# Kernel tuning notes

Measured on AMD Instinct MI355X. Metric: run time of the kernel, lower is better.

## Reference

```python
import jax, jax.numpy as jnp
import numpy as np

B, Q, N_WAY, K_SHOT = 2, 75, 5, 5
C, H, W = 640, 5, 5
PROJ, HEAD_DIM = 640, 32
NUM_HEAD = PROJ // HEAD_DIM
SCALE = HEAD_DIM ** 0.5
TEMP = 12.5
ALPHAS = [2.0 ** k for k in range(-3, 2)]  # cfg.model.mmd.alphas**k, k in [-3,2)


def setup_inputs() -> dict:
    key = jax.random.key(0)
    ks = jax.random.split(key, 7)
    std = (2.0 / PROJ) ** 0.5  # torch init: normal(0, sqrt(2/(k*k*out)))
    return {
        "support_xf": jax.random.normal(ks[0], (B, N_WAY * K_SHOT, C, H, W), jnp.float32),
        "support_y": jax.random.randint(ks[1], (B, N_WAY * K_SHOT), 0, N_WAY),
        "query_xf": jax.random.normal(ks[2], (B, Q, C, H, W), jnp.float32),
        "query_y": jax.random.randint(ks[3], (B, Q), 0, N_WAY),
        "Wq": jax.random.normal(ks[4], (PROJ, C), jnp.float32) * std,
        "Wk": jax.random.normal(ks[5], (PROJ, C), jnp.float32) * std,
        "Wv": jax.random.normal(ks[6], (C, C), jnp.float32) * ((2.0 / C) ** 0.5),
    }


def _qkv(x, Wq, Wk, Wv):
    # x: [b, n, c, h, w]; 1x1 convs == channel matmuls
    b, n, c, h, w = x.shape
    xf = x.reshape(b, n, c, h * w)
    proj = lambda Wm: jnp.einsum('oc,bncp->bnop', Wm, xf)
    k = proj(Wk).reshape(b, n, NUM_HEAD, -1, h * w)                   # [b,n,nh,hd,p]
    q = proj(Wq).reshape(b, n, NUM_HEAD, -1, h * w).swapaxes(-1, -2)  # [b,n,nh,p,hd]
    v = proj(Wv).reshape(b, n, NUM_HEAD, -1, h * w).swapaxes(-1, -2)  # [b,n,nh,p,ch]
    return q, k, v


def _cross_attn(q, k, v, shortcut, dim):
    # q:[b,*,*,nh,p,hd], k:[b,*,*,nh,hd,p], v:[b,*,*,nh,p,ch] (broadcasting over q/s axes)
    attn = jax.nn.softmax((q / SCALE) @ k, axis=-1)
    out = attn @ v                                  # [b,Q,S,nh,p,ch]
    b, nq, s = out.shape[:3]
    h, w = shortcut.shape[-2:]
    out = out.swapaxes(-1, -2).reshape(b, nq, s, -1, h, w)  # [b,Q,S,c,h,w]
    return out + jnp.expand_dims(shortcut, dim)


def _sqdist(x, y):
    # squared euclidean pairwise distances over last-two dims; == cdist(x,y)**2
    xx = jnp.sum(x * x, -1)[..., :, None]
    yy = jnp.sum(y * y, -1)[..., None, :]
    d2 = xx + yy - 2.0 * jnp.einsum('...nc,...mc->...nm', x, y)
    return jnp.maximum(d2, 0.0)


def _mgk(d2):
    # multi-scale gaussian kernel: sum_a exp(-a * dist^2)
    k = jnp.exp(-ALPHAS[0] * d2)
    for a in ALPHAS[1:]:
        k = k + jnp.exp(-a * d2)
    return k


def _forward(support_xf, query_xf, query_y, Wq, Wk, Wv):
    b, q, c, h, w = query_xf.shape
    sq, sk, sv = _qkv(support_xf, Wq, Wk, Wv)
    qq_, qk_, qv_ = _qkv(query_xf, Wq, Wk, Wv)
    # support features attended by query queries (shortcut = support, broadcast over q)
    sbq = _cross_attn(qq_[:, :, None], sk[:, None], sv[:, None], support_xf, dim=1)  # [b,q,s,c,h,w]
    # query features attended by support queries (shortcut = query, broadcast over s)
    qbs = _cross_attn(sq[:, None], qk_[:, :, None], qv_[:, :, None], query_xf, dim=2)

    def regroup(t):  # [b,q,s,c,h,w] -> [b,q,n_way,k_shot*h*w,c]
        t = t.reshape(b, q, N_WAY, K_SHOT, c, h, w)
        return t.transpose(0, 1, 2, 3, 5, 6, 4).reshape(b, q, N_WAY, K_SHOT * h * w, c)

    sxf = regroup(sbq)
    qxf = regroup(qbs)
    # centering over channel dim
    sxf = sxf - sxf.mean(-1, keepdims=True)
    qxf = qxf - qxf.mean(-1, keepdims=True)

    Kss = _mgk(_sqdist(sxf, sxf))  # [b,q,n_way,N,N]
    Kqq = _mgk(_sqdist(qxf, qxf))
    Kqs = _mgk(_sqdist(sxf, qxf))

    N = K_SHOT * h * w  # num features per class-group (== num_fea_per_img)
    tot = lambda K: jnp.sum(K, (-1, -2))
    tr = lambda K: jnp.trace(K, axis1=-2, axis2=-1)  # diagonal removal (::N+1 stride)
    mmd = (tot(Kss) - tr(Kss)) / (N * (N - 1)) \
        + (tot(Kqq) - tr(Kqq)) / (N * (N - 1)) \
        - (2.0 / (N * N)) * tot(Kqs)
    mmd_dis = mmd.reshape(b * q, N_WAY)

    logp = jax.nn.log_softmax(-mmd_dis / TEMP, axis=-1)
    y = query_y.reshape(-1)
    loss = -jnp.mean(jnp.take_along_axis(logp, y[:, None], axis=1))
    return loss


def reference(support_xf, support_y, query_xf, query_y, Wq, Wk, Wv):
    return _forward(support_xf, query_xf, query_y, Wq, Wk, Wv)
```

## Files before the change

kernel.cpp:

```cpp
#include <hip/hip_runtime.h>
#include <math.h>

#define PP    25
#define CCH   640
#define NCOL  5000
#define SCALE_INV 0.17677669529663687f

#define XTB_OFF   0L
#define WB_OFF    1600000L
#define PROJB_OFF 2214400L
#define MMD_OFF   7014400L
#define ONES_OFF  7015168L
#define FEAT_OFF  7015360L
#define FEAT_PER_WAY_US 160000L
#define FEAT_PER_PAIR_US 800000L

typedef __attribute__((ext_vector_type(8)))  short          s16x8;
typedef __attribute__((ext_vector_type(8)))  unsigned short u16x8;
typedef __attribute__((ext_vector_type(4)))  unsigned short u16x4;
typedef __attribute__((ext_vector_type(16))) float          f32x16;

typedef __attribute__((address_space(1))) const unsigned int glb_u32;
typedef __attribute__((address_space(3))) unsigned int       lds_u32;

__device__ inline unsigned short f2bf(float x) {
  unsigned u = __float_as_uint(x);
  unsigned r = u + 0x7fff + ((u >> 16) & 1);
  return (unsigned short)(r >> 16);
}
__device__ inline float bf2f(unsigned short b) {
  return __uint_as_float(((unsigned)b) << 16);
}
__device__ inline unsigned cvtpk(float lo, float hi) {
  unsigned r;
  asm("v_cvt_pk_bf16_f32 %0, %1, %2" : "=v"(r) : "v"(lo), "v"(hi));
  return r;
}

__global__ __launch_bounds__(256) void t_kernel(const float* __restrict__ sup,
                                                const float* __restrict__ qry,
                                                unsigned short* __restrict__ XTB) {
  __shared__ float lds[16000];
  int item = blockIdx.x;
  const float* src = (item < 50) ? (sup + item * 16000) : (qry + (item - 50) * 16000);
  int tid = threadIdx.x;
  for (int e = tid * 4; e < 16000; e += 1024)
    *(float4*)&lds[e] = *(const float4*)&src[e];
  __syncthreads();
  int ibase = item * PP;
  for (int e = tid * 4; e < 16000; e += 1024) {
    int p = e / CCH, c = e - p * CCH;
    u16x4 b;
    b.x = f2bf(lds[(c + 0) * PP + p]);
    b.y = f2bf(lds[(c + 1) * PP + p]);
    b.z = f2bf(lds[(c + 2) * PP + p]);
    b.w = f2bf(lds[(c + 3) * PP + p]);
    *(u16x4*)&XTB[(long)(ibase + p) * CCH + c] = b;
  }
}

__global__ __launch_bounds__(256) void w_kernel(const float* __restrict__ Wq,
                                                const float* __restrict__ Wk,
                                                const float* __restrict__ Wv,
                                                unsigned short* __restrict__ WB,
                                                unsigned short* __restrict__ ones) {
  if (blockIdx.x == 0 && threadIdx.x < 384)
    ones[threadIdx.x] = (threadIdx.x < 64) ? (unsigned short)0x3F80 : (unsigned short)0;
  long base = ((long)blockIdx.x * 256 + threadIdx.x) * 8;
  int m = (int)(base / 409600L);
  long off = base - (long)m * 409600L;
  const float* W = (m == 0) ? Wq : ((m == 1) ? Wk : Wv);
  float4 a = *(const float4*)&W[off];
  float4 c = *(const float4*)&W[off + 4];
  u16x8 v;
  v[0] = f2bf(a.x); v[1] = f2bf(a.y); v[2] = f2bf(a.z); v[3] = f2bf(a.w);
  v[4] = f2bf(c.x); v[5] = f2bf(c.y); v[6] = f2bf(c.z); v[7] = f2bf(c.w);
  *(u16x8*)&WB[base] = v;
}

__global__ __launch_bounds__(512) void proj_kernel(const unsigned short* __restrict__ WB,
                                                   const unsigned short* __restrict__ XTB,
                                                   unsigned short* __restrict__ proj) {
  __shared__ __align__(16) unsigned short At[128 * 64];
  __shared__ __align__(16) unsigned short Bt[128 * 64];
  int m = blockIdx.z;
  int ctile = blockIdx.x * 128, otile = blockIdx.y * 128;
  const unsigned short* Wsrc = WB + (long)m * 409600L;
  unsigned short* out = proj + (long)m * NCOL * CCH;
  int tid = threadIdx.x;
  int w = tid >> 6, lane = tid & 63;
  int wr = w >> 2, wc = w & 3;
  int lr = lane & 31, ksel = lane >> 5;
  int sr = tid >> 2, sg = (tid & 3) * 2;

  f32x16 acc[2];
#pragma unroll
  for (int a = 0; a < 2; a++)
#pragma unroll
    for (int e = 0; e < 16; e++) acc[a][e] = 0.f;

  int bcol = ctile + sr;
  const unsigned short* asrc = Wsrc + (long)(otile + sr) * CCH + sg * 8;
  const unsigned short* bsrc = XTB + (long)bcol * CCH + sg * 8;

  u16x8 pa[2], pb[2];
#pragma unroll
  for (int gi = 0; gi < 2; gi++) {
    pa[gi] = *(const u16x8*)&asrc[gi * 8];
    if (bcol < NCOL) pb[gi] = *(const u16x8*)&bsrc[gi * 8];
    else { u16x8 z; for (int e = 0; e < 8; e++) z[e] = 0; pb[gi] = z; }
  }

  for (int kc = 0; kc < 10; kc++) {
    __syncthreads();
#pragma unroll
    for (int gi = 0; gi < 2; gi++) {
      int g = sg + gi;
      *(u16x8*)&At[sr * 64 + ((g ^ (sr & 7)) << 3)] = pa[gi];
      *(u16x8*)&Bt[sr * 64 + ((g ^ (sr & 7)) << 3)] = pb[gi];
    }
    if (kc < 9) {
      const unsigned short* an = asrc + (kc + 1) * 64;
      const unsigned short* bn = bsrc + (kc + 1) * 64;
#pragma unroll
      for (int gi = 0; gi < 2; gi++) {
        pa[gi] = *(const u16x8*)&an[gi * 8];
        if (bcol < NCOL) pb[gi] = *(const u16x8*)&bn[gi * 8];
      }
    }
    __syncthreads();
#pragma unroll
    for (int ks = 0; ks < 4; ks++) {
      int gk = ks * 2 + ksel;
      s16x8 bf1;
      {
        int R = wc * 32 + lr;
        bf1 = *(const s16x8*)&Bt[R * 64 + ((gk ^ (R & 7)) << 3)];
      }
#pragma unroll
      for (int a = 0; a < 2; a++) {
        int R = (wr + 2 * a) * 32 + lr;
        s16x8 af = *(const s16x8*)&At[R * 64 + ((gk ^ (R & 7)) << 3)];
        acc[a] = __builtin_amdgcn_mfma_f32_32x32x16_bf16(af, bf1, acc[a], 0, 0, 0);
      }
    }
  }

  int col = ctile + wc * 32 + lr;
  if (col < NCOL) {
#pragma unroll
    for (int a = 0; a < 2; a++) {
      int obase = otile + (wr + 2 * a) * 32 + 4 * ksel;
#pragma unroll
      for (int g2 = 0; g2 < 4; g2++) {
        u16x4 v;
        v.x = f2bf(acc[a][g2 * 4 + 0]);
        v.y = f2bf(acc[a][g2 * 4 + 1]);
        v.z = f2bf(acc[a][g2 * 4 + 2]);
        v.w = f2bf(acc[a][g2 * 4 + 3]);
        *(u16x4*)&out[(long)col * CCH + obase + g2 * 8] = v;
      }
    }
  }
}

__global__ __launch_bounds__(256) void attn_kernel(const unsigned short* __restrict__ proj,
                                                   const unsigned short* __restrict__ XTB,
                                                   unsigned short* __restrict__ feat,
                                                   int chunk_start) {
  int tid = threadIdx.x, wid = tid >> 6, lane = tid & 63;
  int lr = lane & 31, hf = lane >> 5;
  int rclamp = lr > 24 ? 24 : lr;
  int bid = blockIdx.x;
  int pw = bid / 10, grp = bid - pw * 10;
  int unit = grp * 4 + wid;
  int side = unit >= 20 ? 1 : 0;
  int head = unit - side * 20;
  int lpi = pw / 5, way = pw - lpi * 5;
  int pair = chunk_start + lpi;
  int b = pair / 75;
  int qcol = (50 + pair) * PP;
  int sitem0 = b * 25 + way * 5;
  int ho = head * 32;
  const unsigned short* Qp = proj;
  const unsigned short* Kp = proj + (long)NCOL * CCH;
  const unsigned short* Vp = proj + 2L * NCOL * CCH;
  unsigned short* fb = feat + (long)pw * FEAT_PER_WAY_US + head * 250 * 32;

  auto ldfrag = [&](const unsigned short* src, int col0, int ks) -> s16x8 {
    return *(const s16x8*)&src[(long)(col0 + rclamp) * CCH + ho + ks * 16 + hf * 8];
  };
  auto ldvfrag = [&](int col0, int ks) -> s16x8 {
    const unsigned short* base = Vp + (long)(col0 + ks * 16 + hf * 8) * CCH + ho + lr;
    s16x8 f;
#pragma unroll
    for (int j = 0; j < 8; j++) f[j] = (short)base[(long)j * CCH];
    return f;
  };

  s16x8 fA0, fA1, fB0, fB1, fV0, fV1;
  float scv[16];
  if (side == 0) {
    fB0 = ldfrag(Qp, qcol, 0); fB1 = ldfrag(Qp, qcol, 1);
  } else {
    fA0 = ldfrag(Kp, qcol, 0); fA1 = ldfrag(Kp, qcol, 1);
    fV0 = ldvfrag(qcol, 0);    fV1 = ldvfrag(qcol, 1);
#pragma unroll
    for (int rg = 0; rg < 16; rg++) {
      int q = (rg & 3) + 8 * (rg >> 2) + 4 * hf;
      int qc = q > 24 ? 24 : q;
      scv[rg] = bf2f(XTB[(long)(qcol + qc) * CCH + ho + lr]);
    }
  }

  for (int shot = 0; shot < 5; shot++) {
    int scol = (sitem0 + shot) * PP;
    s16x8 A0, A1, B0, B1, V0, V1;
    if (side == 0) {
      A0 = ldfrag(Kp, scol, 0); A1 = ldfrag(Kp, scol, 1);
      B0 = fB0; B1 = fB1;
      V0 = ldvfrag(scol, 0);    V1 = ldvfrag(scol, 1);
    } else {
      A0 = fA0; A1 = fA1;
      B0 = ldfrag(Qp, scol, 0); B1 = ldfrag(Qp, scol, 1);
      V0 = fV0; V1 = fV1;
    }
    f32x16 s;
#pragma unroll
    for (int e = 0; e < 16; e++) s[e] = 0.f;
    s = __builtin_amdgcn_mfma_f32_32x32x16_bf16(A0, B0, s, 0, 0, 0);
    s = __builtin_amdgcn_mfma_f32_32x32x16_bf16(A1, B1, s, 0, 0, 0);
    float pv[16];
    float mx = -1e30f;
#pragma unroll
    for (int rg = 0; rg < 16; rg++) {
      int mm = (rg & 3) + 8 * (rg >> 2) + 4 * hf;
      float v = (mm < 25) ? s[rg] : -1e30f;
      pv[rg] = v;
      mx = fmaxf(mx, v);
    }
    mx = fmaxf(mx, __shfl_xor(mx, 32));
    float sum = 0.f;
#pragma unroll
    for (int rg = 0; rg < 16; rg++) {
      float e = __expf((pv[rg] - mx) * SCALE_INV);
      pv[rg] = e;
      sum += e;
    }
    sum += __shfl_xor(sum, 32);
    float rinv = 1.f / sum;
#pragma unroll
    for (int rg = 0; rg < 16; rg++) pv[rg] *= rinv;
    union { unsigned u[4]; s16x8 v; } P0u, P1u;
    {
      float ex[8], fr[8];
#pragma unroll
      for (int r = 0; r < 8; r++) ex[r] = __shfl_xor(pv[r], 32);
#pragma unroll
      for (int j = 0; j < 4; j++) {
        fr[j]     = hf ? ex[4 + j] : pv[j];
        fr[4 + j] = hf ? pv[4 + j] : ex[j];
      }
#pragma unroll
      for (int j = 0; j < 4; j++) P0u.u[j] = cvtpk(fr[2 * j], fr[2 * j + 1]);
#pragma unroll
      for (int r = 0; r < 8; r++) ex[r] = __shfl_xor(pv[8 + r], 32);
#pragma unroll
      for (int j = 0; j < 4; j++) {
        fr[j]     = hf ? ex[4 + j] : pv[8 + j];
        fr[4 + j] = hf ? pv[12 + j] : ex[j];
      }
#pragma unroll
      for (int j = 0; j < 4; j++) P1u.u[j] = cvtpk(fr[2 * j], fr[2 * j + 1]);
    }
    f32x16 o;
#pragma unroll
    for (int e = 0; e < 16; e++) o[e] = 0.f;
    o = __builtin_amdgcn_mfma_f32_32x32x16_bf16(P0u.v, V0, o, 0, 0, 0);
    o = __builtin_amdgcn_mfma_f32_32x32x16_bf16(P1u.v, V1, o, 0, 0, 0);
    unsigned short* frow = fb + (long)((side ? 125 : 0) + shot * 25) * 32;
    const unsigned short* scb = XTB + (long)(scol + 4 * hf) * CCH + ho + lr;
#pragma unroll
    for (int i = 0; i < 8; i++) {
      int rg0 = 2 * i, rg1 = rg0 + 1;
      int qoff = (rg0 & 3) + 8 * (rg0 >> 2);
      int q0 = qoff + 4 * hf, q1 = q0 + 1;
      float sc0, sc1;
      if (side) { sc0 = scv[rg0]; sc1 = scv[rg1]; }
      else {
        sc0 = bf2f(scb[(long)qoff * CCH]);
        sc1 = bf2f(scb[(long)(qoff + 1) * CCH]);
      }
      unsigned u = cvtpk(o[rg0] + sc0, o[rg1] + sc1);
      if (q0 < 25) frow[q0 * 32 + lr] = (unsigned short)u;
      if (q1 < 25) frow[q1 * 32 + lr] = (unsigned short)(u >> 16);
    }
  }
}

__global__ __launch_bounds__(1024) void gram_kernel(const unsigned short* __restrict__ feat,
                                                    const unsigned short* __restrict__ ones,
                                                    float* __restrict__ mmd,
                                                    int chunk_start) {
  __shared__ __align__(16) unsigned short tile[2][16384];
  __shared__ float sums[256], nrmsq[256], meanv[256], nrmv[256];
  __shared__ float red[48];
  int bid = blockIdx.x;
  const unsigned short* fb = feat + (long)bid * FEAT_PER_WAY_US;
  int tid = threadIdx.x;
  int w = tid >> 6, lane = tid & 63;
  int wr = w >> 2, wc = w & 3;
  int lr = lane & 31, ksel = lane >> 5;

  const unsigned short* srcp[2];
  long stepv[2];
#pragma unroll
  for (int i = 0; i < 2; i++) {
    int s = (w * 2 + i) * 64 + lane;
    int row = s >> 3, gs = s & 7, g = gs ^ (row & 7);
    if (row < 250) {
      srcp[i] = fb + (long)((g >> 2) * 250 + row) * 32 + (g & 3) * 8;
      stepv[i] = 16000;
    } else {
      srcp[i] = ones + (row - 250) * 64 + g * 8;
      stepv[i] = 0;
    }
  }

  f32x16 acc[2][2];
#pragma unroll
  for (int a = 0; a < 2; a++)
#pragma unroll
    for (int b2 = 0; b2 < 2; b2++)
#pragma unroll
      for (int e = 0; e < 16; e++) acc[a][b2][e] = 0.f;

#pragma unroll
  for (int i = 0; i < 2; i++)
    __builtin_amdgcn_global_load_lds((glb_u32*)srcp[i],
                                     (lds_u32*)&tile[0][(w * 2 + i) * 512], 16, 0, 0);
  __syncthreads();

  for (int kc = 0; kc < 10; kc++) {
    int cur = kc & 1;
    if (kc < 9) {
#pragma unroll
      for (int i = 0; i < 2; i++)
        __builtin_amdgcn_global_load_lds((glb_u32*)(srcp[i] + (long)(kc + 1) * stepv[i]),
                                         (lds_u32*)&tile[cur ^ 1][(w * 2 + i) * 512], 16, 0, 0);
    }
    const unsigned short* tb = tile[cur];
#pragma unroll
    for (int ks = 0; ks < 4; ks++) {
      int gk = ks * 2 + ksel;
      s16x8 af[2], bfv[2];
#pragma unroll
      for (int a = 0; a < 2; a++) {
        int R = (wr + 4 * a) * 32 + lr;
        af[a] = *(const s16x8*)&tb[R * 64 + ((gk ^ (R & 7)) << 3)];
      }
#pragma unroll
      for (int b2 = 0; b2 < 2; b2++) {
        int R = (wc + 4 * b2) * 32 + lr;
        bfv[b2] = *(const s16x8*)&tb[R * 64 + ((gk ^ (R & 7)) << 3)];
      }
#pragma unroll
      for (int a = 0; a < 2; a++)
#pragma unroll
        for (int b2 = 0; b2 < 2; b2++)
          acc[a][b2] = __builtin_amdgcn_mfma_f32_32x32x16_bf16(af[a], bfv[b2], acc[a][b2], 0, 0, 0);
    }
    __syncthreads();
  }

#pragma unroll
  for (int a = 0; a < 2; a++) {
    int ti = wr + 4 * a;
#pragma unroll
    for (int b2 = 0; b2 < 2; b2++) {
      int tj = wc + 4 * b2;
      int col = tj * 32 + lr;
      if (col == 250) {
#pragma unroll
        for (int rg = 0; rg < 16; rg++) {
          int row = ti * 32 + (rg & 3) + 8 * (rg >> 2) + 4 * ksel;
          if (row < 250) sums[row] = acc[a][b2][rg];
        }
      }
      if (ti == tj) {
#pragma unroll
        for (int rg = 0; rg < 16; rg++) {
          int row = ti * 32 + (rg & 3) + 8 * (rg >> 2) + 4 * ksel;
          if (row == col && row < 250) nrmsq[row] = acc[a][b2][rg];
        }
      }
    }
  }
  __syncthreads();
  if (tid < 250) {
    float s0 = sums[tid];
    float m = s0 * (1.f / 640.f);
    meanv[tid] = m;
    nrmv[tid] = nrmsq[tid] - s0 * m;
  }
  __syncthreads();

  float s_ss = 0.f, s_qq = 0.f, s_x = 0.f;
#pragma unroll
  for (int a = 0; a < 2; a++) {
    int ti = wr + 4 * a;
#pragma unroll
    for (int b2 = 0; b2 < 2; b2++) {
      int tj = wc + 4 * b2;
      int col = tj * 32 + lr;
#pragma unroll
      for (int rg = 0; rg < 16; rg++) {
        int row = ti * 32 + (rg & 3) + 8 * (rg >> 2) + 4 * ksel;
        if (row < 250 && col < 250) {
          float d2 = nrmv[row] + nrmv[col] - 2.f * acc[a][b2][rg]
                   + 1280.f * meanv[row] * meanv[col];
          d2 = fmaxf(d2, 0.f);
          float e = __expf(-0.125f * d2);
          float e2 = e * e, e4 = e2 * e2, e8 = e4 * e4, e16 = e8 * e8;
          float kv = e + e2 + e4 + e8 + e16;
          bool rs = row < 125, cs = col < 125;
          if (rs && cs)        { if (row != col) s_ss += kv; }
          else if (!rs && !cs) { if (row != col) s_qq += kv; }
          else                 s_x += kv;
        }
      }
    }
  }
#pragma unroll
  for (int off = 32; off; off >>= 1) {
    s_ss += __shfl_xor(s_ss, off);
    s_qq += __shfl_xor(s_qq, off);
    s_x  += __shfl_xor(s_x, off);
  }
  if (lane == 0) { red[w * 3] = s_ss; red[w * 3 + 1] = s_qq; red[w * 3 + 2] = s_x; }
  __syncthreads();
  if (tid == 0) {
    float a = 0.f, b2 = 0.f, c = 0.f;
    for (int i = 0; i < 16; i++) { a += red[i * 3]; b2 += red[i * 3 + 1]; c += red[i * 3 + 2]; }
    mmd[(long)chunk_start * 5 + bid] = a * (1.f / 15500.f) + b2 * (1.f / 15500.f) - c * (1.f / 15625.f);
  }
}

__global__ __launch_bounds__(256) void loss_kernel(const float* __restrict__ mmd,
                                                   const int* __restrict__ qy,
                                                   float* __restrict__ out) {
  __shared__ float red[256];
  int tid = threadIdx.x;
  float val = 0.f;
  if (tid < 150) {
    float l[5];
    float mx = -1e30f;
#pragma unroll
    for (int w = 0; w < 5; w++) {
      l[w] = -mmd[tid * 5 + w] * (1.0f / 12.5f);
      mx = fmaxf(mx, l[w]);
    }
    float sum = 0.f;
#pragma unroll
    for (int w = 0; w < 5; w++) sum += __expf(l[w] - mx);
    float lse = mx + logf(sum);
    int y = qy[tid];
    val = -(l[y] - lse);
  }
  red[tid] = val;
  __syncthreads();
  for (int s = 128; s > 0; s >>= 1) {
    if (tid < s) red[tid] += red[tid + s];
    __syncthreads();
  }
  if (tid == 0) out[0] = red[0] * (1.0f / 150.0f);
}

extern "C" void kernel_launch(void* const* d_in, const int* in_sizes, int n_in,
                              void* d_out, int out_size, void* d_ws, size_t ws_size,
                              hipStream_t stream) {
  (void)in_sizes; (void)n_in; (void)out_size;
  const float* sup = (const float*)d_in[0];
  const float* qry = (const float*)d_in[2];
  const int* qy = (const int*)d_in[3];
  const float* Wq = (const float*)d_in[4];
  const float* Wk = (const float*)d_in[5];
  const float* Wv = (const float*)d_in[6];
  float* ws = (float*)d_ws;
  unsigned short* XTB = (unsigned short*)(ws + XTB_OFF);
  unsigned short* WB = (unsigned short*)(ws + WB_OFF);
  unsigned short* projB = (unsigned short*)(ws + PROJB_OFF);
  float* mmd = ws + MMD_OFF;
  unsigned short* ones = (unsigned short*)(ws + ONES_OFF);
  unsigned short* feat = (unsigned short*)(ws + FEAT_OFF);
  float* out = (float*)d_out;

  long wsf = (long)(ws_size / 4);
  long avail_us = (wsf - FEAT_OFF) * 2;
  long chunkL = avail_us / FEAT_PER_PAIR_US;
  int chunk = (chunkL > 150) ? 150 : (chunkL < 1 ? 1 : (int)chunkL);

  hipLaunchKernelGGL(t_kernel, dim3(200), dim3(256), 0, stream, sup, qry, XTB);
  hipLaunchKernelGGL(w_kernel, dim3(600), dim3(256), 0, stream, Wq, Wk, Wv, WB, ones);
  hipLaunchKernelGGL(proj_kernel, dim3(40, 5, 3), dim3(512), 0, stream, WB, XTB, projB);
  for (int c0 = 0; c0 < 150; c0 += chunk) {
    int cp = (150 - c0 < chunk) ? (150 - c0) : chunk;
    hipLaunchKernelGGL(attn_kernel, dim3(cp * 50), dim3(256), 0, stream, projB, XTB, feat, c0);
    hipLaunchKernelGGL(gram_kernel, dim3(cp * 5), dim3(1024), 0, stream, feat, ones, mmd, c0);
  }
  hipLaunchKernelGGL(loss_kernel, dim3(1), dim3(256), 0, stream, mmd, qy, out);
}
```

Before: 260.0 us.

## Pre-transpose V into padded layout and streamline attention softmax

A new vt_kernel transposes the V projection per item into a padded [channel][32-position] bf16 buffer, so the attention kernel loads V MFMA fragments with a single vector load instead of eight strided scalar loads. The softmax drops per-element masking in favour of fixed zeroing of the padded rows, and uses tree reductions. The shuffle-based fragment reshuffle becomes v_permlane32_swap, and normalisation is deferred into the output fma. This costs an extra kernel launch and an extra workspace buffer, which shifts the feature buffer offset and shrinks the available chunk size.

```diff
diff --git a/kernel.cpp b/kernel.cpp
--- a/kernel.cpp
+++ b/kernel.cpp
@@ -4,6 +4,7 @@
 #define PP    25
 #define CCH   640
 #define NCOL  5000
+#define VT2_STRIDE 20480
 #define SCALE_INV 0.17677669529663687f
 
 #define XTB_OFF   0L
@@ -11,7 +12,8 @@
 #define PROJB_OFF 2214400L
 #define MMD_OFF   7014400L
 #define ONES_OFF  7015168L
-#define FEAT_OFF  7015360L
+#define VT2_OFF   7015360L
+#define FEAT_OFF  9063360L
 #define FEAT_PER_WAY_US 160000L
 #define FEAT_PER_PAIR_US 800000L
 
@@ -35,6 +37,9 @@
   unsigned r;
   asm("v_cvt_pk_bf16_f32 %0, %1, %2" : "=v"(r) : "v"(lo), "v"(hi));
   return r;
+}
+__device__ inline void plswap(unsigned &a, unsigned &b) {
+  asm volatile("v_permlane32_swap_b32 %0, %1" : "+v"(a), "+v"(b));
 }
 
 __global__ __launch_bounds__(256) void t_kernel(const float* __restrict__ sup,
@@ -164,7 +169,31 @@
   }
 }
 
+__global__ __launch_bounds__(256) void vt_kernel(const unsigned short* __restrict__ projB,
+                                                 unsigned short* __restrict__ VT2) {
+  __shared__ unsigned short lds[25 * 650];
+  int item = blockIdx.x, tid = threadIdx.x;
+  const unsigned short* src = projB + 2L * NCOL * CCH + (long)item * 25 * CCH;
+  for (int e = tid * 8; e < 16000; e += 2048) {
+    int p = e / 640, o = e - p * 640;
+    *(u16x8*)&lds[p * 650 + o] = *(const u16x8*)&src[p * 640 + o];
+  }
+  __syncthreads();
+  unsigned short* dst = VT2 + (long)item * VT2_STRIDE;
+  for (int e = tid * 8; e < 20480; e += 2048) {
+    int o = e >> 5, pb = e & 31;
+    u16x8 v;
+#pragma unroll
+    for (int j = 0; j < 8; j++) {
+      int p = pb + j;
+      v[j] = (p < 25) ? lds[p * 650 + o] : (unsigned short)0;
+    }
+    *(u16x8*)&dst[e] = v;
+  }
+}
+
 __global__ __launch_bounds__(256) void attn_kernel(const unsigned short* __restrict__ proj,
+                                                   const unsigned short* __restrict__ VT2,
                                                    const unsigned short* __restrict__ XTB,
                                                    unsigned short* __restrict__ feat,
                                                    int chunk_start) {
@@ -179,23 +208,19 @@
   int lpi = pw / 5, way = pw - lpi * 5;
   int pair = chunk_start + lpi;
   int b = pair / 75;
-  int qcol = (50 + pair) * PP;
+  int qitem = 50 + pair;
+  int qcol = qitem * PP;
   int sitem0 = b * 25 + way * 5;
   int ho = head * 32;
   const unsigned short* Qp = proj;
   const unsigned short* Kp = proj + (long)NCOL * CCH;
-  const unsigned short* Vp = proj + 2L * NCOL * CCH;
   unsigned short* fb = feat + (long)pw * FEAT_PER_WAY_US + head * 250 * 32;
 
   auto ldfrag = [&](const unsigned short* src, int col0, int ks) -> s16x8 {
     return *(const s16x8*)&src[(long)(col0 + rclamp) * CCH + ho + ks * 16 + hf * 8];
   };
-  auto ldvfrag = [&](int col0, int ks) -> s16x8 {
-    const unsigned short* base = Vp + (long)(col0 + ks * 16 + hf * 8) * CCH + ho + lr;
-    s16x8 f;
-#pragma unroll
-    for (int j = 0; j < 8; j++) f[j] = (short)base[(long)j * CCH];
-    return f;
+  auto ldvfrag = [&](int item, int ks) -> s16x8 {
+    return *(const s16x8*)&VT2[(long)item * VT2_STRIDE + (ho + lr) * 32 + ks * 16 + hf * 8];
   };
 
   s16x8 fA0, fA1, fB0, fB1, fV0, fV1;
@@ -204,7 +229,7 @@
     fB0 = ldfrag(Qp, qcol, 0); fB1 = ldfrag(Qp, qcol, 1);
   } else {
     fA0 = ldfrag(Kp, qcol, 0); fA1 = ldfrag(Kp, qcol, 1);
-    fV0 = ldvfrag(qcol, 0);    fV1 = ldvfrag(qcol, 1);
+    fV0 = ldvfrag(qitem, 0);   fV1 = ldvfrag(qitem, 1);
 #pragma unroll
     for (int rg = 0; rg < 16; rg++) {
       int q = (rg & 3) + 8 * (rg >> 2) + 4 * hf;
@@ -214,12 +239,12 @@
   }
 
   for (int shot = 0; shot < 5; shot++) {
-    int scol = (sitem0 + shot) * PP;
+    int sitem = sitem0 + shot, scol = sitem * PP;
     s16x8 A0, A1, B0, B1, V0, V1;
     if (side == 0) {
       A0 = ldfrag(Kp, scol, 0); A1 = ldfrag(Kp, scol, 1);
       B0 = fB0; B1 = fB1;
-      V0 = ldvfrag(scol, 0);    V1 = ldvfrag(scol, 1);
+      V0 = ldvfrag(sitem, 0);   V1 = ldvfrag(sitem, 1);
     } else {
       A0 = fA0; A1 = fA1;
       B0 = ldfrag(Qp, scol, 0); B1 = ldfrag(Qp, scol, 1);
@@ -230,48 +255,38 @@
     for (int e = 0; e < 16; e++) s[e] = 0.f;
     s = __builtin_amdgcn_mfma_f32_32x32x16_bf16(A0, B0, s, 0, 0, 0);
     s = __builtin_amdgcn_mfma_f32_32x32x16_bf16(A1, B1, s, 0, 0, 0);
+    float t8[8];
+#pragma unroll
+    for (int i = 0; i < 8; i++) t8[i] = fmaxf(s[i], s[i + 8]);
+#pragma unroll
+    for (int i = 0; i < 4; i++) t8[i] = fmaxf(t8[i], t8[i + 4]);
+    float mx = fmaxf(fmaxf(t8[0], t8[1]), fmaxf(t8[2], t8[3]));
+    mx = fmaxf(mx, __shfl_xor(mx, 32));
     float pv[16];
-    float mx = -1e30f;
-#pragma unroll
-    for (int rg = 0; rg < 16; rg++) {
-      int mm = (rg & 3) + 8 * (rg >> 2) + 4 * hf;
-      float v = (mm < 25) ? s[rg] : -1e30f;
-      pv[rg] = v;
-      mx = fmaxf(mx, v);
-    }
-    mx = fmaxf(mx, __shfl_xor(mx, 32));
-    float sum = 0.f;
-#pragma unroll
-    for (int rg = 0; rg < 16; rg++) {
-      float e = __expf((pv[rg] - mx) * SCALE_INV);
-      pv[rg] = e;
-      sum += e;
-    }
+#pragma unroll
+    for (int rg = 0; rg < 16; rg++) pv[rg] = __expf((s[rg] - mx) * SCALE_INV);
+    pv[13] = 0.f; pv[14] = 0.f; pv[15] = 0.f;
+    if (hf) pv[12] = 0.f;
+    float s8[8];
+#pragma unroll
+    for (int i = 0; i < 8; i++) s8[i] = pv[i] + pv[i + 8];
+#pragma unroll
+    for (int i = 0; i < 4; i++) s8[i] = s8[i] + s8[i + 4];
+    float sum = (s8[0] + s8[1]) + (s8[2] + s8[3]);
     sum += __shfl_xor(sum, 32);
     float rinv = 1.f / sum;
-#pragma unroll
-    for (int rg = 0; rg < 16; rg++) pv[rg] *= rinv;
     union { unsigned u[4]; s16x8 v; } P0u, P1u;
     {
-      float ex[8], fr[8];
-#pragma unroll
-      for (int r = 0; r < 8; r++) ex[r] = __shfl_xor(pv[r], 32);
-#pragma unroll
-      for (int j = 0; j < 4; j++) {
-        fr[j]     = hf ? ex[4 + j] : pv[j];
-        fr[4 + j] = hf ? pv[4 + j] : ex[j];
-      }
-#pragma unroll
-      for (int j = 0; j < 4; j++) P0u.u[j] = cvtpk(fr[2 * j], fr[2 * j + 1]);
-#pragma unroll
-      for (int r = 0; r < 8; r++) ex[r] = __shfl_xor(pv[8 + r], 32);
-#pragma unroll
-      for (int j = 0; j < 4; j++) {
-        fr[j]     = hf ? ex[4 + j] : pv[8 + j];
-        fr[4 + j] = hf ? pv[12 + j] : ex[j];
-      }
-#pragma unroll
-      for (int j = 0; j < 4; j++) P1u.u[j] = cvtpk(fr[2 * j], fr[2 * j + 1]);
+      unsigned a0 = cvtpk(pv[0], pv[1]),  a1 = cvtpk(pv[2], pv[3]);
+      unsigned a2 = cvtpk(pv[4], pv[5]),  a3 = cvtpk(pv[6], pv[7]);
+      plswap(a2, a0);
+      plswap(a3, a1);
+      P0u.u[0] = a0; P0u.u[1] = a1; P0u.u[2] = a2; P0u.u[3] = a3;
+      unsigned b0 = cvtpk(pv[8], pv[9]),   b1 = cvtpk(pv[10], pv[11]);
+      unsigned b2 = cvtpk(pv[12], pv[13]), b3 = cvtpk(pv[14], pv[15]);
+      plswap(b2, b0);
+      plswap(b3, b1);
+      P1u.u[0] = b0; P1u.u[1] = b1; P1u.u[2] = b2; P1u.u[3] = b3;
     }
     f32x16 o;
 #pragma unroll
@@ -291,7 +306,7 @@
         sc0 = bf2f(scb[(long)qoff * CCH]);
         sc1 = bf2f(scb[(long)(qoff + 1) * CCH]);
       }
-      unsigned u = cvtpk(o[rg0] + sc0, o[rg1] + sc1);
+      unsigned u = cvtpk(fmaf(o[rg0], rinv, sc0), fmaf(o[rg1], rinv, sc1));
       if (q0 < 25) frow[q0 * 32 + lr] = (unsigned short)u;
       if (q1 < 25) frow[q1 * 32 + lr] = (unsigned short)(u >> 16);
     }
@@ -492,6 +507,7 @@
   unsigned short* projB = (unsigned short*)(ws + PROJB_OFF);
   float* mmd = ws + MMD_OFF;
   unsigned short* ones = (unsigned short*)(ws + ONES_OFF);
+  unsigned short* VT2 = (unsigned short*)(ws + VT2_OFF);
   unsigned short* feat = (unsigned short*)(ws + FEAT_OFF);
   float* out = (float*)d_out;
 
@@ -503,9 +519,10 @@
   hipLaunchKernelGGL(t_kernel, dim3(200), dim3(256), 0, stream, sup, qry, XTB);
   hipLaunchKernelGGL(w_kernel, dim3(600), dim3(256), 0, stream, Wq, Wk, Wv, WB, ones);
   hipLaunchKernelGGL(proj_kernel, dim3(40, 5, 3), dim3(512), 0, stream, WB, XTB, projB);
+  hipLaunchKernelGGL(vt_kernel, dim3(200), dim3(256), 0, stream, projB, VT2);
   for (int c0 = 0; c0 < 150; c0 += chunk) {
     int cp = (150 - c0 < chunk) ? (150 - c0) : chunk;
-    hipLaunchKernelGGL(attn_kernel, dim3(cp * 50), dim3(256), 0, stream, projB, XTB, feat, c0);
+    hipLaunchKernelGGL(attn_kernel, dim3(cp * 50), dim3(256), 0, stream, projB, VT2, XTB, feat, c0);
     hipLaunchKernelGGL(gram_kernel, dim3(cp * 5), dim3(1024), 0, stream, feat, ones, mmd, c0);
   }
   hipLaunchKernelGGL(loss_kernel, dim3(1), dim3(256), 0, stream, mmd, qy, out);
```

Measured after the change: 298.2 us. 14.7% more time.
